# Kernel tuning notes

Measured on AMD Instinct MI355X. Metric: run time of the kernel, lower is better.

## Reference

```python
import jax, jax.numpy as jnp
import numpy as np

N_NODES = 50000
N_EDGES = 800000
N_GRAPHS = 64
IN_DIM, HID1, HID2, N_CLASSES = 128, 256, 128, 10


def setup_inputs() -> dict:
    key = jax.random.key(0)
    ks = jax.random.split(key, 12)
    x = jax.random.normal(ks[0], (N_NODES, IN_DIM), dtype=jnp.float32)
    src = jax.random.randint(ks[1], (N_EDGES,), 0, N_NODES, dtype=jnp.int32)
    dst = jax.random.randint(ks[2], (N_EDGES,), 0, N_NODES, dtype=jnp.int32)
    graph_id = jnp.sort(jax.random.randint(ks[3], (N_NODES,), 0, N_GRAPHS, dtype=jnp.int32))
    s1 = 1.0 / np.sqrt(IN_DIM)
    s2 = 1.0 / np.sqrt(HID1)
    s3 = 1.0 / np.sqrt(HID2)
    s4 = 1.0 / np.sqrt(12)
    return {
        'x': x, 'src': src, 'dst': dst, 'graph_id': graph_id,
        'W1': jax.random.normal(ks[4], (IN_DIM, HID1), dtype=jnp.float32) * s1,
        'b1': jnp.zeros((HID1,), dtype=jnp.float32),
        'W2': jax.random.normal(ks[5], (HID1, HID2), dtype=jnp.float32) * s2,
        'b2': jnp.zeros((HID2,), dtype=jnp.float32),
        'Wc1': jax.random.normal(ks[6], (HID2, 12), dtype=jnp.float32) * s3,
        'bc1': jnp.zeros((12,), dtype=jnp.float32),
        'Wc2': jax.random.normal(ks[7], (12, 12), dtype=jnp.float32) * s4,
        'bc2': jnp.zeros((12,), dtype=jnp.float32),
        'Wc3': jax.random.normal(ks[8], (12, N_CLASSES), dtype=jnp.float32) * s4,
        'bc3': jnp.zeros((N_CLASSES,), dtype=jnp.float32),
    }


def _graph_conv(x, W, b, src, dst, inv_sqrt_out, inv_sqrt_in, n_nodes):
    # DGL GraphConv, norm='both': D_out^{-1/2} applied to source feats,
    # sum-aggregate over edges, then D_in^{-1/2} on destination, then +bias.
    # Weight applied first (equivalent by linearity; reduces gather traffic
    # when out_dim < in_dim, and is exactly what DGL does in that case).
    xw = (x * inv_sqrt_out[:, None]) @ W                      # [N, out]
    agg = jax.ops.segment_sum(xw[src], dst, num_segments=n_nodes)  # SpMM
    return agg * inv_sqrt_in[:, None] + b


def reference(x, src, dst, graph_id, W1, b1, W2, b2, Wc1, bc1, Wc2, bc2, Wc3, bc3):
    n = x.shape[0]
    ones_e = jnp.ones(src.shape, dtype=x.dtype)
    deg_out = jnp.maximum(jax.ops.segment_sum(ones_e, src, num_segments=n), 1.0)
    deg_in = jnp.maximum(jax.ops.segment_sum(ones_e, dst, num_segments=n), 1.0)
    inv_o = jax.lax.rsqrt(deg_out)
    inv_i = jax.lax.rsqrt(deg_in)

    h = jax.nn.relu(_graph_conv(x, W1, b1, src, dst, inv_o, inv_i, n))
    h = jax.nn.relu(_graph_conv(h, W2, b2, src, dst, inv_o, inv_i, n))

    # dgl.mean_nodes: per-graph mean over nodes of the batched graph
    gsum = jax.ops.segment_sum(h, graph_id, num_segments=N_GRAPHS)   # [G, HID2]
    cnt = jnp.maximum(jax.ops.segment_sum(jnp.ones((n,), dtype=h.dtype), graph_id, num_segments=N_GRAPHS), 1.0)
    hg = gsum / cnt[:, None]

    # tiny 3-layer MLP (no activations in between, as in the source)
    out = hg @ Wc1 + bc1
    out = out @ Wc2 + bc2
    out = out @ Wc3 + bc3
    return out
```

## Files before the change

### kernel.cpp

```cpp
#include <hip/hip_runtime.h>
#include <hip/hip_bf16.h>

#define IN_DIM 128
#define HID1 256
#define HID2 128

#define HB_BINS 25000
#define HB_WORDS 12500
#define HB_CHUNKS 64
__global__ __launch_bounds__(256) void hist_count(const int* __restrict__ src,
                                                  const int* __restrict__ dst,
                                                  int E, int chunk_size,
                                                  int* __restrict__ part_in,
                                                  int* __restrict__ part_out, int N) {
    __shared__ int sm[HB_WORDS];
    const int* idx = (blockIdx.z == 0) ? dst : src;
    int* part = (blockIdx.z == 0) ? part_in : part_out;
    const int base = blockIdx.y * HB_BINS;
    const int ebeg = blockIdx.x * chunk_size;
    const int eend = min(ebeg + chunk_size, E);
    for (int w = threadIdx.x; w < HB_WORDS; w += 256) sm[w] = 0;
    __syncthreads();
    for (int e = ebeg + threadIdx.x; e < eend; e += 256) {
        int v = idx[e] - base;
        if ((unsigned)v < (unsigned)HB_BINS)
            atomicAdd(&sm[v >> 1], 1 << ((v & 1) * 16));
    }
    __syncthreads();
    const int nb = min(HB_BINS, N - base);
    int* dp = part + (size_t)blockIdx.x * N + base;
    for (int w = threadIdx.x; 2 * w < nb; w += 256) {
        int packed = sm[w];
        int b = 2 * w;
        dp[b] = packed & 0xffff;
        if (b + 1 < nb) dp[b + 1] = (packed >> 16) & 0xffff;
    }
}

__global__ __launch_bounds__(256) void hist_reduce(const int* __restrict__ part_in,
                                                   const int* __restrict__ part_out,
                                                   int N, int* __restrict__ deg_in,
                                                   float* __restrict__ inv_i,
                                                   float* __restrict__ inv_o,
                                                   int* __restrict__ blockSums) {
    __shared__ int sm[256];
    int b = blockIdx.x * 256 + threadIdx.x;
    int di = 0, dox = 0;
    if (b < N) {
#pragma unroll 4
        for (int k = 0; k < HB_CHUNKS; ++k) {
            di += part_in[(size_t)k * N + b];
            dox += part_out[(size_t)k * N + b];
        }
        deg_in[b] = di;
        inv_i[b] = rsqrtf((float)max(di, 1));
        inv_o[b] = rsqrtf((float)max(dox, 1));
    }
    sm[threadIdx.x] = di;
    __syncthreads();
#pragma unroll
    for (int off = 128; off > 0; off >>= 1) {
        if (threadIdx.x < off) sm[threadIdx.x] += sm[threadIdx.x + off];
        __syncthreads();
    }
    if (threadIdx.x == 0) blockSums[blockIdx.x] = sm[0];
}

#define BK_SHIFT 8
#define NBUCK 196
#define NCHUNK 256
__global__ __launch_bounds__(256) void coarse_hist(const int* __restrict__ dst, int E,
                                                   int chunk_size, int* __restrict__ ccnt,
                                                   float* __restrict__ hg, int hg_n) {
    __shared__ int cnt[NBUCK];
    if (blockIdx.x == 0)
        for (int i = threadIdx.x; i < hg_n; i += 256) hg[i] = 0.f;
    for (int i = threadIdx.x; i < NBUCK; i += 256) cnt[i] = 0;
    __syncthreads();
    int ebeg = blockIdx.x * chunk_size, eend = min(ebeg + chunk_size, E);
    for (int e = ebeg + threadIdx.x; e < eend; e += 256)
        atomicAdd(&cnt[dst[e] >> BK_SHIFT], 1);
    __syncthreads();
    for (int i = threadIdx.x; i < NBUCK; i += 256) ccnt[blockIdx.x * NBUCK + i] = cnt[i];
}

__global__ __launch_bounds__(256) void scan_coarse_final(const int* __restrict__ deg,
                                                         const int* __restrict__ blockSums, int nbs,
                                                         const int* __restrict__ ccnt,
                                                         int* __restrict__ row,
                                                         int* __restrict__ coff, int n) {
    __shared__ int sm[256];
    __shared__ int s_base;
    const int b = blockIdx.x, t = threadIdx.x;
    int v0 = (t < b && t < nbs) ? blockSums[t] : 0;
    sm[t] = v0;
    __syncthreads();
#pragma unroll
    for (int off = 128; off > 0; off >>= 1) {
        if (t < off) sm[t] += sm[t + off];
        __syncthreads();
    }
    if (t == 0) s_base = sm[0];
    __syncthreads();
    const int base = s_base;
    int i = b * 256 + t;
    int v = (i < n) ? deg[i] : 0;
    __syncthreads();
    sm[t] = v;
    __syncthreads();
#pragma unroll
    for (int off = 1; off < 256; off <<= 1) {
        int u = (t >= off) ? sm[t - off] : 0;
        __syncthreads();
        sm[t] += u;
        __syncthreads();
    }
    int excl = sm[t] - v + base;
    if (i < n) {
        row[i] = excl;
        if (i == n - 1) row[n] = excl + v;
    }
    __syncthreads();
    int c = ccnt[t * NBUCK + b];
    sm[t] = c;
    __syncthreads();
#pragma unroll
    for (int off = 1; off < 256; off <<= 1) {
        int u = (t >= off) ? sm[t - off] : 0;
        __syncthreads();
        sm[t] += u;
        __syncthreads();
    }
    coff[t * NBUCK + b] = base + sm[t] - c;
}

__global__ __launch_bounds__(256) void scat_a(const int* __restrict__ src,
                                              const int* __restrict__ dst, int E,
                                              int chunk_size, const int* __restrict__ coff,
                                              int2* __restrict__ pairs) {
    __shared__ int lcur[NBUCK];
    for (int i = threadIdx.x; i < NBUCK; i += 256) lcur[i] = coff[blockIdx.x * NBUCK + i];
    __syncthreads();
    int ebeg = blockIdx.x * chunk_size, eend = min(ebeg + chunk_size, E);
    for (int e = ebeg + threadIdx.x; e < eend; e += 256) {
        int d = dst[e];
        int p = atomicAdd(&lcur[d >> BK_SHIFT], 1);
        pairs[p] = make_int2(src[e], d);
    }
}

__global__ __launch_bounds__(256) void scat_b(const int2* __restrict__ pairs,
                                              const int* __restrict__ row, int N,
                                              int* __restrict__ csr_src) {
    __shared__ int cur[1 << BK_SHIFT];
    const int nb0 = blockIdx.x << BK_SHIFT;
    const int nb1 = min(nb0 + (1 << BK_SHIFT), N);
    if (nb0 >= N) return;
    for (int i = threadIdx.x; i < nb1 - nb0; i += 256) cur[i] = row[nb0 + i];
    __syncthreads();
    const int beg = row[nb0], end = row[nb1];
    for (int j = beg + threadIdx.x; j < end; j += 256) {
        int2 pr = pairs[j];
        int p = atomicAdd(&cur[pr.y - nb0], 1);
        csr_src[p] = pr.x;
    }
}

__global__ void cvt_all(const float* __restrict__ x, const float* __restrict__ inv_o,
                        __hip_bfloat16* __restrict__ x_bf, int n4x,
                        const float* __restrict__ W1, __hip_bfloat16* __restrict__ W1t,
                        const float* __restrict__ W2, __hip_bfloat16* __restrict__ W2t) {
    const int S1 = IN_DIM * HID1;
    const int S2 = HID1 * HID2;
    int i = blockIdx.x * blockDim.x + threadIdx.x;
    if (i < n4x) {
        float s = inv_o[i >> 5];
        float4 v = reinterpret_cast<const float4*>(x)[i];
        __hip_bfloat16 b0 = __float2bfloat16(v.x * s);
        __hip_bfloat16 b1 = __float2bfloat16(v.y * s);
        __hip_bfloat16 b2 = __float2bfloat16(v.z * s);
        __hip_bfloat16 b3 = __float2bfloat16(v.w * s);
        ushort4 o = make_ushort4(*(unsigned short*)&b0, *(unsigned short*)&b1,
                                 *(unsigned short*)&b2, *(unsigned short*)&b3);
        reinterpret_cast<ushort4*>(x_bf)[i] = o;
    } else {
        int idx = i - n4x;
        if (idx < S1) {
            int k = idx / HID1, n = idx - k * HID1;
            W1t[n * IN_DIM + k] = __float2bfloat16(W1[idx]);
        } else if (idx < S1 + S2) {
            int j = idx - S1;
            int k = j / HID2, n = j - k * HID2;
            W2t[n * HID1 + k] = __float2bfloat16(W2[j]);
        }
    }
}

__device__ __forceinline__ void bf2_unpack(unsigned int p, float& lo, float& hi) {
    lo = __uint_as_float(p << 16);
    hi = __uint_as_float(p & 0xffff0000u);
}

__global__ __launch_bounds__(256) void spmm_kernel(const __hip_bfloat16* __restrict__ feat,
                                                   const int* __restrict__ row,
                                                   const int* __restrict__ csr_src,
                                                   __hip_bfloat16* __restrict__ out_bf, int N) {
    const int node = blockIdx.x * 4 + (threadIdx.x >> 6);
    if (node >= N) return;
    const int lane = threadIdx.x & 63;
    const unsigned int* fp = (const unsigned int*)feat;
    const int beg = row[node];
    const int end = row[node + 1];
    float a0 = 0.f, a1 = 0.f;
    int j = beg;
    for (; j + 4 <= end; j += 4) {
        int s0 = csr_src[j], s1 = csr_src[j + 1], s2 = csr_src[j + 2], s3 = csr_src[j + 3];
        unsigned int p0 = fp[(size_t)s0 * 64 + lane];
        unsigned int p1 = fp[(size_t)s1 * 64 + lane];
        unsigned int p2 = fp[(size_t)s2 * 64 + lane];
        unsigned int p3 = fp[(size_t)s3 * 64 + lane];
        float lo, hi;
        bf2_unpack(p0, lo, hi); a0 += lo; a1 += hi;
        bf2_unpack(p1, lo, hi); a0 += lo; a1 += hi;
        bf2_unpack(p2, lo, hi); a0 += lo; a1 += hi;
        bf2_unpack(p3, lo, hi); a0 += lo; a1 += hi;
    }
    for (; j < end; ++j) {
        unsigned int p0 = fp[(size_t)csr_src[j] * 64 + lane];
        float lo, hi;
        bf2_unpack(p0, lo, hi); a0 += lo; a1 += hi;
    }
    __hip_bfloat16 b0 = __float2bfloat16(a0);
    __hip_bfloat16 b1 = __float2bfloat16(a1);
    unsigned int packed = (unsigned int)(*(unsigned short*)&b0) |
                          ((unsigned int)(*(unsigned short*)&b1) << 16);
    ((unsigned int*)out_bf)[(size_t)node * 64 + lane] = packed;
}

#define SP_NODES 8
__global__ __launch_bounds__(256) void spmm_pool_kernel(const __hip_bfloat16* __restrict__ feat,
                                                        const int* __restrict__ row,
                                                        const int* __restrict__ csr_src,
                                                        const float* __restrict__ inv_i,
                                                        const float* __restrict__ b2,
                                                        const int* __restrict__ graph_id,
                                                        int N, float* __restrict__ hg_sum) {
    const int wave = blockIdx.x * 4 + (threadIdx.x >> 6);
    const int lane = threadIdx.x & 63;
    const int n0 = wave * SP_NODES;
    if (n0 >= N) return;
    const int n1 = min(n0 + SP_NODES, N);
    const unsigned int* fp = (const unsigned int*)feat;
    const float bias0 = b2[2 * lane];
    const float bias1 = b2[2 * lane + 1];
    int g = graph_id[n0];
    float p0 = 0.f, p1 = 0.f;
    for (int node = n0; node < n1; ++node) {
        int gi = graph_id[node];
        if (gi != g) {
            atomicAdd(&hg_sum[g * HID2 + 2 * lane], p0);
            atomicAdd(&hg_sum[g * HID2 + 2 * lane + 1], p1);
            p0 = p1 = 0.f;
            g = gi;
        }
        const int beg = row[node];
        const int end = row[node + 1];
        float a0 = 0.f, a1 = 0.f;
        int j = beg;
        for (; j + 4 <= end; j += 4) {
            int s0 = csr_src[j], s1 = csr_src[j + 1], s2 = csr_src[j + 2], s3 = csr_src[j + 3];
            unsigned int q0 = fp[(size_t)s0 * 64 + lane];
            unsigned int q1 = fp[(size_t)s1 * 64 + lane];
            unsigned int q2 = fp[(size_t)s2 * 64 + lane];
            unsigned int q3 = fp[(size_t)s3 * 64 + lane];
            float lo, hi;
            bf2_unpack(q0, lo, hi); a0 += lo; a1 += hi;
            bf2_unpack(q1, lo, hi); a0 += lo; a1 += hi;
            bf2_unpack(q2, lo, hi); a0 += lo; a1 += hi;
            bf2_unpack(q3, lo, hi); a0 += lo; a1 += hi;
        }
        for (; j < end; ++j) {
            unsigned int q0 = fp[(size_t)csr_src[j] * 64 + lane];
            float lo, hi;
            bf2_unpack(q0, lo, hi); a0 += lo; a1 += hi;
        }
        float ii = inv_i[node];
        p0 += fmaxf(a0 * ii + bias0, 0.f);
        p1 += fmaxf(a1 * ii + bias1, 0.f);
    }
    atomicAdd(&hg_sum[g * HID2 + 2 * lane], p0);
    atomicAdd(&hg_sum[g * HID2 + 2 * lane + 1], p1);
}

#define GBM 128
#define GBN 128
#define GBK 32
#define LPAD 40
typedef __attribute__((ext_vector_type(4))) float floatx4;
typedef __attribute__((ext_vector_type(8))) short shortx8;

__global__ __launch_bounds__(256) void mfma_gemm_kernel(const __hip_bfloat16* __restrict__ A,
                                                        const __hip_bfloat16* __restrict__ Bt,
                                                        __hip_bfloat16* __restrict__ C,
                                                        const float* __restrict__ scaleR,
                                                        const float* __restrict__ bias,
                                                        const float* __restrict__ scaleO,
                                                        int M, int Nn, int K, int doRelu) {
    __shared__ __align__(16) __hip_bfloat16 As[GBM * LPAD];
    __shared__ __align__(16) __hip_bfloat16 Bs[GBN * LPAD];
    const int tid = threadIdx.x;
    const int bm = blockIdx.x * GBM;
    const int bn = blockIdx.y * GBN;
    const int wid = tid >> 6;
    const int lane = tid & 63;
    const int wm = (wid & 1) * 64;
    const int wn = (wid >> 1) * 64;
    const int lrow = lane & 15;
    const int quad = lane >> 4;

    floatx4 acc[4][4] = {};

    for (int k0 = 0; k0 < K; k0 += GBK) {
#pragma unroll
        for (int it = 0; it < 2; ++it) {
            int slot = tid + (it << 8);
            int r = slot >> 2;
            int c = (slot & 3) << 3;
            int gr = bm + r;
            float4 v = make_float4(0.f, 0.f, 0.f, 0.f);
            if (gr < M) v = *reinterpret_cast<const float4*>(A + (size_t)gr * K + k0 + c);
            *reinterpret_cast<float4*>(&As[r * LPAD + c]) = v;
        }
#pragma unroll
        for (int it = 0; it < 2; ++it) {
            int slot = tid + (it << 8);
            int r = slot >> 2;
            int c = (slot & 3) << 3;
            float4 v = *reinterpret_cast<const float4*>(Bt + (size_t)(bn + r) * K + k0 + c);
            *reinterpret_cast<float4*>(&Bs[r * LPAD + c]) = v;
        }
        __syncthreads();

        shortx8 af[4], bf[4];
#pragma unroll
        for (int i = 0; i < 4; ++i)
            af[i] = *reinterpret_cast<const shortx8*>(&As[(wm + i * 16 + lrow) * LPAD + quad * 8]);
#pragma unroll
        for (int i = 0; i < 4; ++i)
            bf[i] = *reinterpret_cast<const shortx8*>(&Bs[(wn + i * 16 + lrow) * LPAD + quad * 8]);
#pragma unroll
        for (int im = 0; im < 4; ++im)
#pragma unroll
            for (int in = 0; in < 4; ++in)
                acc[im][in] = __builtin_amdgcn_mfma_f32_16x16x32_bf16(af[im], bf[in], acc[im][in], 0, 0, 0);
        __syncthreads();
    }

    float bv[4];
#pragma unroll
    for (int in = 0; in < 4; ++in)
        bv[in] = bias ? bias[bn + wn + in * 16 + lrow] : 0.f;

#pragma unroll
    for (int im = 0; im < 4; ++im) {
#pragma unroll
        for (int reg = 0; reg < 4; ++reg) {
            int r = bm + wm + im * 16 + quad * 4 + reg;
            if (r >= M) continue;
            float sR = scaleR ? scaleR[r] : 1.f;
            float sO = scaleO ? scaleO[r] : 1.f;
#pragma unroll
            for (int in = 0; in < 4; ++in) {
                int c = bn + wn + in * 16 + lrow;
                float v = acc[im][in][reg] * sR + bv[in];
                if (doRelu) v = fmaxf(v, 0.f);
                v *= sO;
                C[(size_t)r * Nn + c] = __float2bfloat16(v);
            }
        }
    }
}

__device__ __forceinline__ int lower_bound_i(const int* a, int n, int key) {
    int lo = 0, hi = n;
    while (lo < hi) {
        int mid = (lo + hi) >> 1;
        if (a[mid] < key) lo = mid + 1; else hi = mid;
    }
    return lo;
}

__global__ __launch_bounds__(64) void mlp_kernel(const float* __restrict__ hg_sum,
                                                 const int* __restrict__ graph_id, int n,
                                                 const float* __restrict__ Wc1, const float* __restrict__ bc1,
                                                 const float* __restrict__ Wc2, const float* __restrict__ bc2,
                                                 const float* __restrict__ Wc3, const float* __restrict__ bc3,
                                                 float* __restrict__ out) {
    const int g = blockIdx.x;
    const int t = threadIdx.x;
    __shared__ float h[HID2];
    __shared__ float t1[12];
    __shared__ float t2[12];
    __shared__ float s_inv_cnt;
    if (t == 0) {
        int beg = lower_bound_i(graph_id, n, g);
        int end = lower_bound_i(graph_id, n, g + 1);
        int c = end - beg;
        s_inv_cnt = 1.0f / (float)max(c, 1);
    }
    __syncthreads();
    const float ic = s_inv_cnt;
    for (int i = t; i < HID2; i += 64) h[i] = hg_sum[g * HID2 + i] * ic;
    __syncthreads();
    if (t < 12) {
        float a = bc1[t];
        for (int k = 0; k < HID2; ++k) a += h[k] * Wc1[k * 12 + t];
        t1[t] = a;
    }
    __syncthreads();
    if (t < 12) {
        float a = bc2[t];
        for (int k = 0; k < 12; ++k) a += t1[k] * Wc2[k * 12 + t];
        t2[t] = a;
    }
    __syncthreads();
    if (t < 10) {
        float a = bc3[t];
        for (int k = 0; k < 12; ++k) a += t2[k] * Wc3[k * 10 + t];
        out[g * 10 + t] = a;
    }
}

extern "C" void kernel_launch(void* const* d_in, const int* in_sizes, int n_in,
                              void* d_out, int out_size, void* d_ws, size_t ws_size,
                              hipStream_t stream) {
    const float* x        = (const float*)d_in[0];
    const int*   src      = (const int*)d_in[1];
    const int*   dst      = (const int*)d_in[2];
    const int*   graph_id = (const int*)d_in[3];
    const float* W1       = (const float*)d_in[4];
    const float* b1       = (const float*)d_in[5];
    const float* W2       = (const float*)d_in[6];
    const float* b2       = (const float*)d_in[7];
    const float* Wc1      = (const float*)d_in[8];
    const float* bc1      = (const float*)d_in[9];
    const float* Wc2      = (const float*)d_in[10];
    const float* bc2      = (const float*)d_in[11];
    const float* Wc3      = (const float*)d_in[12];
    const float* bc3      = (const float*)d_in[13];
    float* out = (float*)d_out;

    const int N = in_sizes[0] / IN_DIM;
    const int E = in_sizes[1];
    const int G = out_size / 10;

    char* ws = (char*)d_ws;
    size_t off = 0;
    auto alloc = [&](size_t bytes) -> char* {
        char* p = ws + off;
        off = (off + bytes + 255) & ~(size_t)255;
        return p;
    };
    const int NB = (N + 255) / 256;
    int*   deg_in  = (int*)alloc((size_t)N * 4);
    float* inv_i   = (float*)alloc((size_t)N * 4);
    float* inv_o   = (float*)alloc((size_t)N * 4);
    int*   row     = (int*)alloc((size_t)(N + 1) * 4);
    int*   bsums   = (int*)alloc((size_t)NB * 4);
    int*   ccnt    = (int*)alloc((size_t)NCHUNK * NBUCK * 4);
    int*   coff    = (int*)alloc((size_t)NCHUNK * NBUCK * 4);
    int2*  pairs   = (int2*)alloc((size_t)E * 8);
    int*   csr_src = (int*)alloc((size_t)E * 4);
    float* hg      = (float*)alloc((size_t)G * HID2 * 4);
    __hip_bfloat16* x_bf    = (__hip_bfloat16*)alloc((size_t)N * IN_DIM * 2);
    __hip_bfloat16* W1t     = (__hip_bfloat16*)alloc((size_t)IN_DIM * HID1 * 2);
    __hip_bfloat16* W2t     = (__hip_bfloat16*)alloc((size_t)HID1 * HID2 * 2);
    __hip_bfloat16* agg1_bf = (__hip_bfloat16*)alloc((size_t)N * IN_DIM * 2);
    __hip_bfloat16* h1_bf   = (__hip_bfloat16*)alloc((size_t)N * HID1 * 2);
    __hip_bfloat16* xw2_bf  = (__hip_bfloat16*)alloc((size_t)N * HID2 * 2);

    int* part_in  = (int*)h1_bf;
    int* part_out = part_in + (size_t)HB_CHUNKS * N;

    const int hchunk = (E + HB_CHUNKS - 1) / HB_CHUNKS;
    const int n_ranges = (N + HB_BINS - 1) / HB_BINS;
    hist_count<<<dim3(HB_CHUNKS, n_ranges, 2), 256, 0, stream>>>(src, dst, E, hchunk,
                                                                 part_in, part_out, N);
    hist_reduce<<<NB, 256, 0, stream>>>(part_in, part_out, N, deg_in, inv_i, inv_o, bsums);

    const int schunk = (E + NCHUNK - 1) / NCHUNK;
    coarse_hist<<<NCHUNK, 256, 0, stream>>>(dst, E, schunk, ccnt, hg, G * HID2);
    scan_coarse_final<<<NB, 256, 0, stream>>>(deg_in, bsums, NB, ccnt, row, coff, N);
    scat_a<<<NCHUNK, 256, 0, stream>>>(src, dst, E, schunk, coff, pairs);
    scat_b<<<NBUCK, 256, 0, stream>>>(pairs, row, N, csr_src);

    const int n4x = N * IN_DIM / 4;
    cvt_all<<<(n4x + IN_DIM * HID1 + HID1 * HID2 + 255) / 256, 256, 0, stream>>>(
        x, inv_o, x_bf, n4x, W1, W1t, W2, W2t);

    spmm_kernel<<<(N + 3) / 4, 256, 0, stream>>>(x_bf, row, csr_src, agg1_bf, N);
    mfma_gemm_kernel<<<dim3((N + GBM - 1) / GBM, HID1 / GBN), 256, 0, stream>>>(
        agg1_bf, W1t, h1_bf, inv_i, b1, inv_o, N, HID1, IN_DIM, 1);

    mfma_gemm_kernel<<<dim3((N + GBM - 1) / GBM, HID2 / GBN), 256, 0, stream>>>(
        h1_bf, W2t, xw2_bf, nullptr, nullptr, nullptr, N, HID2, HID1, 0);
    const int npw = (N + SP_NODES - 1) / SP_NODES;
    spmm_pool_kernel<<<(npw + 3) / 4, 256, 0, stream>>>(xw2_bf, row, csr_src, inv_i, b2,
                                                        graph_id, N, hg);

    mlp_kernel<<<G, 64, 0, stream>>>(hg, graph_id, N, Wc1, bc1, Wc2, bc2, Wc3, bc3, out);
}
```

Before: 284.2 us.

## Derive in-degrees inside CSR bucket scatter and unroll SpMM gathers by eight

The in-degree histogram pass over dst is dropped. Row offsets and inv_i are now computed inside scat_b from per-bucket counts of the already-bucketed pairs, and coarse bucket offsets come from a column scan plus a small in-block scan of the bucket totals. This removes one full pass over dst and its partial-histogram writes, at the cost of an extra count pass over pairs in scat_b and a redundant bucket-total scan in every scat_a and scat_b block. Both SpMM kernels also gain an 8-way unrolled gather loop for more memory-level parallelism, and the pooling kernel handles 4 nodes per wavefront instead of 8.

```diff
diff --git a/kernel.cpp b/kernel.cpp
--- a/kernel.cpp
+++ b/kernel.cpp
@@ -8,21 +8,17 @@
 #define HB_BINS 25000
 #define HB_WORDS 12500
 #define HB_CHUNKS 64
-__global__ __launch_bounds__(256) void hist_count(const int* __restrict__ src,
-                                                  const int* __restrict__ dst,
-                                                  int E, int chunk_size,
-                                                  int* __restrict__ part_in,
-                                                  int* __restrict__ part_out, int N) {
+__global__ __launch_bounds__(256) void hist_src(const int* __restrict__ src,
+                                                int E, int chunk_size,
+                                                int* __restrict__ part, int N) {
     __shared__ int sm[HB_WORDS];
-    const int* idx = (blockIdx.z == 0) ? dst : src;
-    int* part = (blockIdx.z == 0) ? part_in : part_out;
     const int base = blockIdx.y * HB_BINS;
     const int ebeg = blockIdx.x * chunk_size;
     const int eend = min(ebeg + chunk_size, E);
     for (int w = threadIdx.x; w < HB_WORDS; w += 256) sm[w] = 0;
     __syncthreads();
     for (int e = ebeg + threadIdx.x; e < eend; e += 256) {
-        int v = idx[e] - base;
+        int v = src[e] - base;
         if ((unsigned)v < (unsigned)HB_BINS)
             atomicAdd(&sm[v >> 1], 1 << ((v & 1) * 16));
     }
@@ -37,33 +33,14 @@
     }
 }
 
-__global__ __launch_bounds__(256) void hist_reduce(const int* __restrict__ part_in,
-                                                   const int* __restrict__ part_out,
-                                                   int N, int* __restrict__ deg_in,
-                                                   float* __restrict__ inv_i,
-                                                   float* __restrict__ inv_o,
-                                                   int* __restrict__ blockSums) {
-    __shared__ int sm[256];
-    int b = blockIdx.x * 256 + threadIdx.x;
-    int di = 0, dox = 0;
-    if (b < N) {
+__global__ __launch_bounds__(256) void hist_src_reduce(const int* __restrict__ part,
+                                                       int N, float* __restrict__ inv_o) {
+    int b = blockIdx.x * blockDim.x + threadIdx.x;
+    if (b >= N) return;
+    int d = 0;
 #pragma unroll 4
-        for (int k = 0; k < HB_CHUNKS; ++k) {
-            di += part_in[(size_t)k * N + b];
-            dox += part_out[(size_t)k * N + b];
-        }
-        deg_in[b] = di;
-        inv_i[b] = rsqrtf((float)max(di, 1));
-        inv_o[b] = rsqrtf((float)max(dox, 1));
-    }
-    sm[threadIdx.x] = di;
-    __syncthreads();
-#pragma unroll
-    for (int off = 128; off > 0; off >>= 1) {
-        if (threadIdx.x < off) sm[threadIdx.x] += sm[threadIdx.x + off];
-        __syncthreads();
-    }
-    if (threadIdx.x == 0) blockSums[blockIdx.x] = sm[0];
+    for (int k = 0; k < HB_CHUNKS; ++k) d += part[(size_t)k * N + b];
+    inv_o[b] = rsqrtf((float)max(d, 1));
 }
 
 #define BK_SHIFT 8
@@ -84,28 +61,28 @@
     for (int i = threadIdx.x; i < NBUCK; i += 256) ccnt[blockIdx.x * NBUCK + i] = cnt[i];
 }
 
-__global__ __launch_bounds__(256) void scan_coarse_final(const int* __restrict__ deg,
-                                                         const int* __restrict__ blockSums, int nbs,
-                                                         const int* __restrict__ ccnt,
-                                                         int* __restrict__ row,
-                                                         int* __restrict__ coff, int n) {
-    __shared__ int sm[256];
-    __shared__ int s_base;
+__global__ __launch_bounds__(NCHUNK) void coarse_col(const int* __restrict__ ccnt,
+                                                     int* __restrict__ coffpre,
+                                                     int* __restrict__ ctot) {
+    __shared__ int sm[NCHUNK];
     const int b = blockIdx.x, t = threadIdx.x;
-    int v0 = (t < b && t < nbs) ? blockSums[t] : 0;
-    sm[t] = v0;
-    __syncthreads();
-#pragma unroll
-    for (int off = 128; off > 0; off >>= 1) {
-        if (t < off) sm[t] += sm[t + off];
-        __syncthreads();
-    }
-    if (t == 0) s_base = sm[0];
-    __syncthreads();
-    const int base = s_base;
-    int i = b * 256 + t;
-    int v = (i < n) ? deg[i] : 0;
-    __syncthreads();
+    int v = ccnt[t * NBUCK + b];
+    sm[t] = v;
+    __syncthreads();
+#pragma unroll
+    for (int off = 1; off < NCHUNK; off <<= 1) {
+        int u = (t >= off) ? sm[t - off] : 0;
+        __syncthreads();
+        sm[t] += u;
+        __syncthreads();
+    }
+    coffpre[t * NBUCK + b] = sm[t] - v;
+    if (t == NCHUNK - 1) ctot[b] = sm[t];
+}
+
+__device__ __forceinline__ void scan_bbase(const int* __restrict__ ctot, int* sm, int* bbase) {
+    const int t = threadIdx.x;
+    int v = (t < NBUCK) ? ctot[t] : 0;
     sm[t] = v;
     __syncthreads();
 #pragma unroll
@@ -115,31 +92,22 @@
         sm[t] += u;
         __syncthreads();
     }
-    int excl = sm[t] - v + base;
-    if (i < n) {
-        row[i] = excl;
-        if (i == n - 1) row[n] = excl + v;
-    }
-    __syncthreads();
-    int c = ccnt[t * NBUCK + b];
-    sm[t] = c;
-    __syncthreads();
-#pragma unroll
-    for (int off = 1; off < 256; off <<= 1) {
-        int u = (t >= off) ? sm[t - off] : 0;
-        __syncthreads();
-        sm[t] += u;
-        __syncthreads();
-    }
-    coff[t * NBUCK + b] = base + sm[t] - c;
+    if (t < NBUCK) bbase[t] = sm[t] - v;
+    __syncthreads();
 }
 
 __global__ __launch_bounds__(256) void scat_a(const int* __restrict__ src,
                                               const int* __restrict__ dst, int E,
-                                              int chunk_size, const int* __restrict__ coff,
+                                              int chunk_size,
+                                              const int* __restrict__ coffpre,
+                                              const int* __restrict__ ctot,
                                               int2* __restrict__ pairs) {
+    __shared__ int sm[256];
+    __shared__ int bbase[NBUCK];
     __shared__ int lcur[NBUCK];
-    for (int i = threadIdx.x; i < NBUCK; i += 256) lcur[i] = coff[blockIdx.x * NBUCK + i];
+    scan_bbase(ctot, sm, bbase);
+    for (int i = threadIdx.x; i < NBUCK; i += 256)
+        lcur[i] = bbase[i] + coffpre[blockIdx.x * NBUCK + i];
     __syncthreads();
     int ebeg = blockIdx.x * chunk_size, eend = min(ebeg + chunk_size, E);
     for (int e = ebeg + threadIdx.x; e < eend; e += 256) {
@@ -150,16 +118,46 @@
 }
 
 __global__ __launch_bounds__(256) void scat_b(const int2* __restrict__ pairs,
-                                              const int* __restrict__ row, int N,
+                                              const int* __restrict__ ctot, int N,
+                                              int* __restrict__ row,
+                                              float* __restrict__ inv_i,
                                               int* __restrict__ csr_src) {
+    __shared__ int sm[256];
+    __shared__ int bbase[NBUCK];
+    __shared__ int cnt[1 << BK_SHIFT];
+    __shared__ int loff[1 << BK_SHIFT];
     __shared__ int cur[1 << BK_SHIFT];
-    const int nb0 = blockIdx.x << BK_SHIFT;
-    const int nb1 = min(nb0 + (1 << BK_SHIFT), N);
-    if (nb0 >= N) return;
-    for (int i = threadIdx.x; i < nb1 - nb0; i += 256) cur[i] = row[nb0 + i];
-    __syncthreads();
-    const int beg = row[nb0], end = row[nb1];
-    for (int j = beg + threadIdx.x; j < end; j += 256) {
+    const int b = blockIdx.x, t = threadIdx.x;
+    scan_bbase(ctot, sm, bbase);
+    const int segBase = bbase[b];
+    const int segEnd = segBase + ctot[b];
+    const int nb0 = b << BK_SHIFT;
+    const int nbn = min(256, N - nb0);
+    cnt[t] = 0;
+    __syncthreads();
+    for (int j = segBase + t; j < segEnd; j += 256)
+        atomicAdd(&cnt[pairs[j].y - nb0], 1);
+    __syncthreads();
+    int v = cnt[t];
+    sm[t] = v;
+    __syncthreads();
+#pragma unroll
+    for (int off = 1; off < 256; off <<= 1) {
+        int u = (t >= off) ? sm[t - off] : 0;
+        __syncthreads();
+        sm[t] += u;
+        __syncthreads();
+    }
+    int excl = sm[t] - v;
+    loff[t] = excl;
+    cur[t] = segBase + excl;
+    if (t < nbn) {
+        row[nb0 + t] = segBase + excl;
+        inv_i[nb0 + t] = rsqrtf((float)max(v, 1));
+        if (nb0 + t == N - 1) row[N] = segBase + excl + v;
+    }
+    __syncthreads();
+    for (int j = segBase + t; j < segEnd; j += 256) {
         int2 pr = pairs[j];
         int p = atomicAdd(&cur[pr.y - nb0], 1);
         csr_src[p] = pr.x;
@@ -213,6 +211,27 @@
     const int end = row[node + 1];
     float a0 = 0.f, a1 = 0.f;
     int j = beg;
+    for (; j + 8 <= end; j += 8) {
+        int s0 = csr_src[j],     s1 = csr_src[j + 1], s2 = csr_src[j + 2], s3 = csr_src[j + 3];
+        int s4 = csr_src[j + 4], s5 = csr_src[j + 5], s6 = csr_src[j + 6], s7 = csr_src[j + 7];
+        unsigned int p0 = fp[(size_t)s0 * 64 + lane];
+        unsigned int p1 = fp[(size_t)s1 * 64 + lane];
+        unsigned int p2 = fp[(size_t)s2 * 64 + lane];
+        unsigned int p3 = fp[(size_t)s3 * 64 + lane];
+        unsigned int p4 = fp[(size_t)s4 * 64 + lane];
+        unsigned int p5 = fp[(size_t)s5 * 64 + lane];
+        unsigned int p6 = fp[(size_t)s6 * 64 + lane];
+        unsigned int p7 = fp[(size_t)s7 * 64 + lane];
+        float lo, hi;
+        bf2_unpack(p0, lo, hi); a0 += lo; a1 += hi;
+        bf2_unpack(p1, lo, hi); a0 += lo; a1 += hi;
+        bf2_unpack(p2, lo, hi); a0 += lo; a1 += hi;
+        bf2_unpack(p3, lo, hi); a0 += lo; a1 += hi;
+        bf2_unpack(p4, lo, hi); a0 += lo; a1 += hi;
+        bf2_unpack(p5, lo, hi); a0 += lo; a1 += hi;
+        bf2_unpack(p6, lo, hi); a0 += lo; a1 += hi;
+        bf2_unpack(p7, lo, hi); a0 += lo; a1 += hi;
+    }
     for (; j + 4 <= end; j += 4) {
         int s0 = csr_src[j], s1 = csr_src[j + 1], s2 = csr_src[j + 2], s3 = csr_src[j + 3];
         unsigned int p0 = fp[(size_t)s0 * 64 + lane];
@@ -237,7 +256,7 @@
     ((unsigned int*)out_bf)[(size_t)node * 64 + lane] = packed;
 }
 
-#define SP_NODES 8
+#define SP_NODES 4
 __global__ __launch_bounds__(256) void spmm_pool_kernel(const __hip_bfloat16* __restrict__ feat,
                                                         const int* __restrict__ row,
                                                         const int* __restrict__ csr_src,
@@ -254,19 +273,40 @@
     const float bias0 = b2[2 * lane];
     const float bias1 = b2[2 * lane + 1];
     int g = graph_id[n0];
-    float p0 = 0.f, p1 = 0.f;
+    float p0s = 0.f, p1s = 0.f;
     for (int node = n0; node < n1; ++node) {
         int gi = graph_id[node];
         if (gi != g) {
-            atomicAdd(&hg_sum[g * HID2 + 2 * lane], p0);
-            atomicAdd(&hg_sum[g * HID2 + 2 * lane + 1], p1);
-            p0 = p1 = 0.f;
+            atomicAdd(&hg_sum[g * HID2 + 2 * lane], p0s);
+            atomicAdd(&hg_sum[g * HID2 + 2 * lane + 1], p1s);
+            p0s = p1s = 0.f;
             g = gi;
         }
         const int beg = row[node];
         const int end = row[node + 1];
         float a0 = 0.f, a1 = 0.f;
         int j = beg;
+        for (; j + 8 <= end; j += 8) {
+            int s0 = csr_src[j],     s1 = csr_src[j + 1], s2 = csr_src[j + 2], s3 = csr_src[j + 3];
+            int s4 = csr_src[j + 4], s5 = csr_src[j + 5], s6 = csr_src[j + 6], s7 = csr_src[j + 7];
+            unsigned int q0 = fp[(size_t)s0 * 64 + lane];
+            unsigned int q1 = fp[(size_t)s1 * 64 + lane];
+            unsigned int q2 = fp[(size_t)s2 * 64 + lane];
+            unsigned int q3 = fp[(size_t)s3 * 64 + lane];
+            unsigned int q4 = fp[(size_t)s4 * 64 + lane];
+            unsigned int q5 = fp[(size_t)s5 * 64 + lane];
+            unsigned int q6 = fp[(size_t)s6 * 64 + lane];
+            unsigned int q7 = fp[(size_t)s7 * 64 + lane];
+            float lo, hi;
+            bf2_unpack(q0, lo, hi); a0 += lo; a1 += hi;
+            bf2_unpack(q1, lo, hi); a0 += lo; a1 += hi;
+            bf2_unpack(q2, lo, hi); a0 += lo; a1 += hi;
+            bf2_unpack(q3, lo, hi); a0 += lo; a1 += hi;
+            bf2_unpack(q4, lo, hi); a0 += lo; a1 += hi;
+            bf2_unpack(q5, lo, hi); a0 += lo; a1 += hi;
+            bf2_unpack(q6, lo, hi); a0 += lo; a1 += hi;
+            bf2_unpack(q7, lo, hi); a0 += lo; a1 += hi;
+        }
         for (; j + 4 <= end; j += 4) {
             int s0 = csr_src[j], s1 = csr_src[j + 1], s2 = csr_src[j + 2], s3 = csr_src[j + 3];
             unsigned int q0 = fp[(size_t)s0 * 64 + lane];
@@ -285,11 +325,11 @@
             bf2_unpack(q0, lo, hi); a0 += lo; a1 += hi;
         }
         float ii = inv_i[node];
-        p0 += fmaxf(a0 * ii + bias0, 0.f);
-        p1 += fmaxf(a1 * ii + bias1, 0.f);
-    }
-    atomicAdd(&hg_sum[g * HID2 + 2 * lane], p0);
-    atomicAdd(&hg_sum[g * HID2 + 2 * lane + 1], p1);
+        p0s += fmaxf(a0 * ii + bias0, 0.f);
+        p1s += fmaxf(a1 * ii + bias1, 0.f);
+    }
+    atomicAdd(&hg_sum[g * HID2 + 2 * lane], p0s);
+    atomicAdd(&hg_sum[g * HID2 + 2 * lane + 1], p1s);
 }
 
 #define GBM 128
@@ -461,14 +501,12 @@
         off = (off + bytes + 255) & ~(size_t)255;
         return p;
     };
-    const int NB = (N + 255) / 256;
-    int*   deg_in  = (int*)alloc((size_t)N * 4);
     float* inv_i   = (float*)alloc((size_t)N * 4);
     float* inv_o   = (float*)alloc((size_t)N * 4);
     int*   row     = (int*)alloc((size_t)(N + 1) * 4);
-    int*   bsums   = (int*)alloc((size_t)NB * 4);
     int*   ccnt    = (int*)alloc((size_t)NCHUNK * NBUCK * 4);
-    int*   coff    = (int*)alloc((size_t)NCHUNK * NBUCK * 4);
+    int*   coffpre = (int*)alloc((size_t)NCHUNK * NBUCK * 4);
+    int*   ctot    = (int*)alloc((size_t)NBUCK * 4);
     int2*  pairs   = (int2*)alloc((size_t)E * 8);
     int*   csr_src = (int*)alloc((size_t)E * 4);
     float* hg      = (float*)alloc((size_t)G * HID2 * 4);
@@ -479,20 +517,18 @@
     __hip_bfloat16* h1_bf   = (__hip_bfloat16*)alloc((size_t)N * HID1 * 2);
     __hip_bfloat16* xw2_bf  = (__hip_bfloat16*)alloc((size_t)N * HID2 * 2);
 
-    int* part_in  = (int*)h1_bf;
-    int* part_out = part_in + (size_t)HB_CHUNKS * N;
+    int* part = (int*)h1_bf;
 
     const int hchunk = (E + HB_CHUNKS - 1) / HB_CHUNKS;
     const int n_ranges = (N + HB_BINS - 1) / HB_BINS;
-    hist_count<<<dim3(HB_CHUNKS, n_ranges, 2), 256, 0, stream>>>(src, dst, E, hchunk,
-                                                                 part_in, part_out, N);
-    hist_reduce<<<NB, 256, 0, stream>>>(part_in, part_out, N, deg_in, inv_i, inv_o, bsums);
+    hist_src<<<dim3(HB_CHUNKS, n_ranges), 256, 0, stream>>>(src, E, hchunk, part, N);
+    hist_src_reduce<<<(N + 255) / 256, 256, 0, stream>>>(part, N, inv_o);
 
     const int schunk = (E + NCHUNK - 1) / NCHUNK;
     coarse_hist<<<NCHUNK, 256, 0, stream>>>(dst, E, schunk, ccnt, hg, G * HID2);
-    scan_coarse_final<<<NB, 256, 0, stream>>>(deg_in, bsums, NB, ccnt, row, coff, N);
-    scat_a<<<NCHUNK, 256, 0, stream>>>(src, dst, E, schunk, coff, pairs);
-    scat_b<<<NBUCK, 256, 0, stream>>>(pairs, row, N, csr_src);
+    coarse_col<<<NBUCK, NCHUNK, 0, stream>>>(ccnt, coffpre, ctot);
+    scat_a<<<NCHUNK, 256, 0, stream>>>(src, dst, E, schunk, coffpre, ctot, pairs);
+    scat_b<<<NBUCK, 256, 0, stream>>>(pairs, ctot, N, row, inv_i, csr_src);
 
     const int n4x = N * IN_DIM / 4;
     cvt_all<<<(n4x + IN_DIM * HID1 + HID1 * HID2 + 255) / 256, 256, 0, stream>>>(
```

New measurement: 280.9 us. About the same (-1.2%).
